# Kernel optimization log

Hardware: AMD Instinct MI355X
Metric: run time of the kernel (lower is better)

Reference implementation:

```python
import jax, jax.numpy as jnp
import numpy as np
from jax import lax

KERNEL = 3      # patch size
STRIDE = 1      # matching stride at low res
RATE = 2        # downsample rate
SOFTMAX_SCALE = 10.0


def _extract_patches(img, k, stride):
    """tf.image.extract_patches with SAME padding. img: [B,H,W,C] -> [B, oh*ow, k, k, C]."""
    B, H, W, C = img.shape
    oh = -(-H // stride)
    ow = -(-W // stride)
    ph = max((oh - 1) * stride + k - H, 0)
    pw = max((ow - 1) * stride + k - W, 0)
    img = jnp.pad(img, ((0, 0), (ph // 2, ph - ph // 2), (pw // 2, pw - pw // 2), (0, 0)))
    # stack the k*k shifted strided views; channel-last order matches TF's (kh, kw, C) flattening
    cols = [img[:, dh:dh + (oh - 1) * stride + 1:stride, dw:dw + (ow - 1) * stride + 1:stride, :]
            for dh in range(k) for dw in range(k)]
    p = jnp.stack(cols, axis=3)  # [B, oh, ow, k*k, C]
    return p.reshape(B, oh * ow, k, k, C)


def _avgpool2(x):
    """Exact equivalent of TF bilinear (antialias=False) downsample by factor 2."""
    B, H, W, C = x.shape
    return x.reshape(B, H // 2, 2, W // 2, 2, C).mean(axis=(2, 4))


def _conv_same(x4, w):
    return lax.conv_general_dilated(x4, w, (1, 1), 'SAME',
                                    dimension_numbers=('NHWC', 'HWIO', 'NHWC'))


def _forward(x, mask):
    B, H, W, C = x.shape
    k, stride, rate = KERNEL, STRIDE, RATE
    h, w = H // rate, W // rate
    L = h * w

    # raw (full-res) patches used for reconstruction: [B,k,k,C,L]
    raw_w = jnp.transpose(_extract_patches(x, k, rate * stride), (0, 2, 3, 4, 1))
    # low-res foreground / background (identical here, as in the source)
    f = _avgpool2(x)              # [B,h,w,C]
    m = _avgpool2(mask)           # [B,h,w,1]
    # low-res matching patches: [B,k,k,C,L]
    wp = jnp.transpose(_extract_patches(f, k, stride), (0, 2, 3, 4, 1))
    # mask patches -> gate: mm = 1 where the 3x3 mask patch mean is exactly 1.0
    mp = _extract_patches(m, k, stride)                       # [B,L,k,k,1]
    mm = (jnp.mean(mp, axis=(2, 3, 4)) == 1.0).astype(jnp.float32)  # [B,L]

    fuse_w = jnp.eye(KERNEL, dtype=jnp.float32).reshape(KERNEL, KERNEL, 1, 1)

    def per_item(xi, wi, rwi, mmi):
        # xi:[h,w,C]  wi,rwi:[k,k,C,L]  mmi:[L]
        wn = wi / jnp.maximum(jnp.sqrt(jnp.sum(wi * wi, axis=(0, 1, 2))), 1e-4)
        yi = _conv_same(xi[None], wn)          # [1,h,w,L] cosine-similarity logits
        att = yi[0]
        # fuse: diagonal conv over the [L,L] score matrix in both patch orderings
        z = yi.reshape(1, L, L, 1)
        z = _conv_same(z, fuse_w)
        z = z.reshape(1, h, w, h, w).transpose(0, 2, 1, 4, 3).reshape(1, L, L, 1)
        z = _conv_same(z, fuse_w)
        z = z.reshape(1, w, h, w, h).transpose(0, 2, 1, 4, 3)
        yi = z.reshape(1, h, w, L)
        mm4 = mmi.reshape(1, 1, 1, L)
        yi = jax.nn.softmax(yi * mm4 * SOFTMAX_SCALE, axis=3) * mm4
        # reconstruction: transposed conv with raw full-res patches as filters
        out = lax.conv_transpose(yi, rwi, (rate, rate), 'SAME',
                                 dimension_numbers=('NHWC', 'HWIO', 'NHWC'),
                                 transpose_kernel=True) / float(rate * rate)
        return out[0], att

    y, att = jax.vmap(per_item)(f, wp, raw_w, mm)
    return y, att


def setup_inputs() -> dict:
    key = jax.random.key(0)
    x = jax.random.normal(key, (2, 128, 128, 64), dtype=jnp.float32)
    # binary hole mask: ones inside a centered 64x64 square
    mask = jnp.zeros((2, 128, 128, 1), jnp.float32).at[:, 32:96, 32:96, :].set(1.0)
    return {"x": x, "mask": mask}


def reference(x, mask):
    return _forward(x, mask)
```

## Files before the change

kernel.cpp:

```cpp
#include <hip/hip_runtime.h>
#include <hip/hip_bf16.h>

typedef _Float16 f16x8 __attribute__((ext_vector_type(8)));
typedef float f32x4 __attribute__((ext_vector_type(4)));

__device__ __forceinline__ void gload_lds16(const void* gptr, void* lptr) {
  __builtin_amdgcn_global_load_lds(
      (const __attribute__((address_space(1))) void*)gptr,
      (__attribute__((address_space(3))) void*)lptr, 16, 0, 0);
}

__global__ __launch_bounds__(256) void k_pre(const float* __restrict__ x,
                                             const float* __restrict__ mask,
                                             _Float16* __restrict__ f_h,
                                             float* __restrict__ sumsq,
                                             float* __restrict__ mlow) {
  int wave = threadIdx.x >> 6, c = threadIdx.x & 63;
  int blk = blockIdx.x * 4 + wave;
  int b = blk >> 12, ij = blk & 4095;
  int i = ij >> 6, j = ij & 63;
  size_t base = ((size_t)(b * 128 + 2 * i) * 128 + 2 * j) * 64 + c;
  float f = 0.25f * (x[base] + x[base + 64] + x[base + 128 * 64] + x[base + 128 * 64 + 64]);
  f_h[(size_t)blk * 64 + c] = (_Float16)f;
  float fsq = f * f;
  for (int off = 32; off; off >>= 1) fsq += __shfl_down(fsq, off);
  if (c == 0) {
    sumsq[blk] = fsq;
    size_t mb = (size_t)(b * 128 + 2 * i) * 128 + 2 * j;
    mlow[blk] = 0.25f * (mask[mb] + mask[mb + 1] + mask[mb + 128] + mask[mb + 129]);
  }
}

__global__ __launch_bounds__(1024) void k_norm_compact(const float* __restrict__ sumsq,
                                                       const float* __restrict__ mlow,
                                                       float* __restrict__ invn,
                                                       int* __restrict__ actIdx,
                                                       int* __restrict__ nAct) {
  int b = blockIdx.x;
  int t = threadIdx.x;
  __shared__ unsigned char mmf[4096];
  for (int l = t; l < 4096; l += 1024) {
    int li = l >> 6, lj = l & 63;
    float s = 0.f;
    bool ok = true;
    for (int dh = -1; dh <= 1; ++dh)
      for (int dw = -1; dw <= 1; ++dw) {
        int ii = li + dh, jj = lj + dw;
        float mv = 0.f;
        if ((unsigned)ii < 64u && (unsigned)jj < 64u) {
          int idx = (b << 12) + ii * 64 + jj;
          s += sumsq[idx];
          mv = mlow[idx];
        }
        ok = ok && (mv == 1.0f);
      }
    invn[(b << 12) + l] = 1.0f / fmaxf(sqrtf(s), 1e-4f);
    mmf[l] = ok ? 1 : 0;
  }
  __syncthreads();
  int lane = t & 63, wv = t >> 6;
  __shared__ int wsum[16];
  __shared__ int sbase;
  if (t == 0) sbase = 0;
  __syncthreads();
  for (int chunk = 0; chunk < 4; ++chunk) {
    int l = chunk * 1024 + t;
    int flag = mmf[l] ? 1 : 0;
    unsigned long long m = __ballot(flag);
    int wpre = __popcll(m & ((1ull << lane) - 1ull));
    if (lane == 0) wsum[wv] = __popcll(m);
    __syncthreads();
    int off = sbase;
    for (int w2 = 0; w2 < wv; ++w2) off += wsum[w2];
    if (flag) {
      int pos = off + wpre;
      if (pos < 1024) actIdx[(b << 10) + pos] = l;
    }
    __syncthreads();
    if (t == 0) {
      int s2 = 0;
      for (int w2 = 0; w2 < 16; ++w2) s2 += wsum[w2];
      sbase += s2;
    }
    __syncthreads();
  }
  int total = sbase;
  if (t >= total) actIdx[(b << 10) + t] = 0;
  if (t == 0) nAct[b] = (total > 1024) ? 1024 : total;
}

__global__ __launch_bounds__(256) void k_build_p(const _Float16* __restrict__ f_h,
                                                 _Float16* __restrict__ P) {
  int wave = threadIdx.x >> 6, c = threadIdx.x & 63;
  int blk = blockIdx.x * 4 + wave;
  int b = blk >> 12, l = blk & 4095;
  int li = l >> 6, lj = l & 63;
  _Float16* dst = P + (size_t)blk * 576 + c;
#pragma unroll
  for (int kk = 0; kk < 9; ++kk) {
    int kh = kk / 3, kw = kk % 3;
    int ii = li + kh - 1, jj = lj + kw - 1;
    _Float16 v = (_Float16)0.f;
    if ((unsigned)ii < 64u && (unsigned)jj < 64u)
      v = f_h[((size_t)(b << 12) + ii * 64 + jj) * 64 + c];
    dst[kk * 64] = v;
  }
}

__global__ void k_build_rt(const float* __restrict__ x, _Float16* __restrict__ Rt) {
  int kh = blockIdx.x, li = blockIdx.y, b = blockIdx.z;
  int r = 2 * li + kh;
  __shared__ float xrow[128 * 65];
  if (r < 128) {
    for (int t = threadIdx.x; t < 8192; t += 256) {
      int v = t >> 6, c = t & 63;
      xrow[v * 65 + c] = x[((size_t)(b * 128 + r) * 128 + v) * 64 + c];
    }
  }
  __syncthreads();
  for (int idx = threadIdx.x; idx < 12288; idx += 256) {
    int lj = idx & 63, rest = idx >> 6;
    int c = rest & 63, kw = rest >> 6;
    int v = 2 * lj + kw;
    float val = (r < 128 && v < 128) ? xrow[v * 65 + c] : 0.f;
    int n = (kh * 3 + kw) * 64 + c;
    Rt[((size_t)b * 640 + n) * 4096 + li * 64 + lj] = (_Float16)val;
  }
}

__global__ void k_rtsub(const _Float16* __restrict__ Rt, const int* __restrict__ actIdx,
                        _Float16* __restrict__ Rts) {
  int n = blockIdx.x, b = blockIdx.y;
  const _Float16* src = Rt + ((size_t)b * 640 + n) * 4096;
  _Float16* dst = Rts + ((size_t)b * 640 + n) * 1024;
  const int* aIdx = actIdx + (b << 10);
  for (int s = threadIdx.x; s < 1024; s += 256) dst[s] = src[aIdx[s]];
}

__global__ __launch_bounds__(256) void k_gemm_sim(const _Float16* __restrict__ P,
                                                  const float* __restrict__ invn,
                                                  float* __restrict__ att) {
  int b = blockIdx.z;
  const _Float16* Ab = P + (size_t)b * 4096 * 576;
  int idx = blockIdx.x;
  int bj = (int)((sqrtf(8.f * (float)idx + 1.f) - 1.f) * 0.5f);
  while ((bj + 1) * (bj + 2) / 2 <= idx) ++bj;
  while (bj * (bj + 1) / 2 > idx) --bj;
  int bi = idx - bj * (bj + 1) / 2;
  int rowBase = bi * 128, colBase = bj * 128;
  bool diag = (bi == bj);

  __shared__ alignas(16) _Float16 As[128 * 64];
  __shared__ alignas(16) _Float16 Bs[128 * 64];
  __shared__ alignas(16) float tbuf[32][132];
  int tid = threadIdx.x, wave = tid >> 6, lane = tid & 63;
  int q = lane >> 4, rr = lane & 15;
  int wr = (wave >> 1) * 64, wc = (wave & 1) * 64;
  f32x4 acc[4][4] = {};
  for (int kt = 0; kt < 576; kt += 64) {
    __syncthreads();
#pragma unroll
    for (int t = 0; t < 4; ++t) {
      int chunk = t * 256 + wave * 64 + lane;
      int row = chunk >> 3;
      int kc = ((chunk & 7) ^ (row & 7)) * 8;
      gload_lds16(Ab + (size_t)(rowBase + row) * 576 + kt + kc,
                  As + (size_t)(t * 256 + wave * 64) * 8);
      if (!diag)
        gload_lds16(Ab + (size_t)(colBase + row) * 576 + kt + kc,
                    Bs + (size_t)(t * 256 + wave * 64) * 8);
    }
    __syncthreads();
    const _Float16* Bsrc = diag ? As : Bs;
#pragma unroll
    for (int ks = 0; ks < 2; ++ks) {
      f16x8 af[4], bf[4];
#pragma unroll
      for (int mi = 0; mi < 4; ++mi) {
        int r = wr + mi * 16 + rr;
        int ps = (ks * 4 + q) ^ (r & 7);
        af[mi] = *(const f16x8*)(As + r * 64 + ps * 8);
      }
#pragma unroll
      for (int ni = 0; ni < 4; ++ni) {
        int r = wc + ni * 16 + rr;
        int ps = (ks * 4 + q) ^ (r & 7);
        bf[ni] = *(const f16x8*)(Bsrc + r * 64 + ps * 8);
      }
#pragma unroll
      for (int mi = 0; mi < 4; ++mi)
#pragma unroll
        for (int ni = 0; ni < 4; ++ni)
          acc[mi][ni] = __builtin_amdgcn_mfma_f32_16x16x32_f16(af[mi], bf[ni], acc[mi][ni], 0, 0, 0);
    }
  }
  float* attb = att + ((size_t)b << 24);
#pragma unroll
  for (int ni = 0; ni < 4; ++ni) {
    int gc = colBase + wc + ni * 16 + rr;
    float sc = invn[(b << 12) + gc];
#pragma unroll
    for (int mi = 0; mi < 4; ++mi)
#pragma unroll
      for (int reg = 0; reg < 4; ++reg) {
        int gr = rowBase + wr + mi * 16 + q * 4 + reg;
        attb[((size_t)gr << 12) + gc] = acc[mi][ni][reg] * sc;
      }
  }
  if (diag) return;
  const float* ivrow = invn + (b << 12) + rowBase;
#pragma unroll
  for (int ph = 0; ph < 4; ++ph) {
    __syncthreads();
    if ((ph >> 1) == (wc >> 6)) {
      int nlo = (ph & 1) * 2;
#pragma unroll
      for (int nn = 0; nn < 2; ++nn) {
        int ni = nlo + nn;
        int rloc = nn * 16 + rr;
#pragma unroll
        for (int mi = 0; mi < 4; ++mi)
          *(f32x4*)&tbuf[rloc][wr + mi * 16 + q * 4] = acc[mi][ni];
      }
    }
    __syncthreads();
    int r = tid >> 3;
    int cbase = (tid & 7) * 16;
    int grow = colBase + ph * 32 + r;
    float* dst = attb + ((size_t)grow << 12) + rowBase + cbase;
#pragma unroll
    for (int cc = 0; cc < 16; cc += 4) {
      f32x4 v = *(f32x4*)&tbuf[r][cbase + cc];
      f32x4 s = *(const f32x4*)(ivrow + cbase + cc);
      *(f32x4*)(dst + cc) = v * s;
    }
  }
}

__global__ __launch_bounds__(256) void k_fuse_softmax3(const float* __restrict__ att,
                                                       const int* __restrict__ actIdx,
                                                       const int* __restrict__ nAct,
                                                       _Float16* __restrict__ Asub) {
  int blk0 = blockIdx.x;
  int blk = (blk0 & 7) * 1024 + (blk0 >> 3);
  int b = blk >> 12, p = blk & 4095;
  const float* Y = att + ((size_t)b << 24);
  const int* aIdx = actIdx + (b << 10);
  int na = nAct[b];
  int tid = threadIdx.x;
  int pi = p >> 6, pj = p & 63;
  int acol = pj * 64 + pi;

  int ls[4];
  bool act[4];
  float F[4] = {0.f, 0.f, 0.f, 0.f};
#pragma unroll
  for (int s4 = 0; s4 < 4; ++s4) {
    int slot = s4 * 256 + tid;
    ls[s4] = aIdx[slot];
    act[s4] = (slot < na);
  }

#pragma unroll
  for (int d2 = -1; d2 <= 1; ++d2) {
    int a2 = acol + d2;
    if ((unsigned)a2 >= 4096u) continue;
    int p2 = ((a2 & 63) << 6) | (a2 >> 6);
    int l2[4];
    bool lok[4];
#pragma unroll
    for (int s4 = 0; s4 < 4; ++s4) {
      int l = ls[s4];
      int bcol = ((l & 63) << 6) | (l >> 6);
      int b2 = bcol + d2;
      lok[s4] = act[s4] && ((unsigned)b2 < 4096u);
      int b2c = lok[s4] ? b2 : 0;
      l2[s4] = ((b2c & 63) << 6) | (b2c >> 6);
    }
#pragma unroll
    for (int d1 = -1; d1 <= 1; ++d1) {
      int qq = p2 + d1;
      if ((unsigned)qq >= 4096u) continue;
      const float* row = Y + ((size_t)qq << 12);
#pragma unroll
      for (int s4 = 0; s4 < 4; ++s4) {
        int rr2 = l2[s4] + d1;
        if (lok[s4] && (unsigned)rr2 < 4096u) F[s4] += row[rr2];
      }
    }
  }

  float z[4];
  float mx = (na < 4096) ? 0.f : -1e30f;
#pragma unroll
  for (int s4 = 0; s4 < 4; ++s4) {
    z[s4] = act[s4] ? F[s4] * 10.f : -1e30f;
    mx = fmaxf(mx, z[s4]);
  }
  __shared__ float red[4];
  for (int off = 32; off; off >>= 1) mx = fmaxf(mx, __shfl_down(mx, off));
  if ((tid & 63) == 0) red[tid >> 6] = mx;
  __syncthreads();
  mx = fmaxf(fmaxf(red[0], red[1]), fmaxf(red[2], red[3]));
  float e[4];
  float esum = 0.f;
#pragma unroll
  for (int s4 = 0; s4 < 4; ++s4) {
    e[s4] = act[s4] ? __expf(z[s4] - mx) : 0.f;
    esum += e[s4];
  }
  for (int off = 32; off; off >>= 1) esum += __shfl_down(esum, off);
  __syncthreads();
  if ((tid & 63) == 0) red[tid >> 6] = esum;
  __syncthreads();
  float total = red[0] + red[1] + red[2] + red[3] + (float)(4096 - na) * __expf(0.f - mx);
  float inv = 1.f / total;
  _Float16* Ap = Asub + ((size_t)blk << 10);
#pragma unroll
  for (int s4 = 0; s4 < 4; ++s4) Ap[s4 * 256 + tid] = (_Float16)(e[s4] * inv);
}

__global__ __launch_bounds__(256) void k_gemm_recon(const _Float16* __restrict__ Asub,
                                                    const _Float16* __restrict__ Rts,
                                                    float* __restrict__ y) {
  int b = blockIdx.z;
  const _Float16* Ab = Asub + ((size_t)b << 22);
  const _Float16* Bb = Rts + (size_t)b * 640 * 1024;
  int rowBase = blockIdx.y * 128, colBase = blockIdx.x * 128;
  __shared__ alignas(16) _Float16 As[128 * 64];
  __shared__ alignas(16) _Float16 Bs[128 * 64];
  int tid = threadIdx.x, wave = tid >> 6, lane = tid & 63;
  int q = lane >> 4, rr = lane & 15;
  int wr = (wave >> 1) * 64, wc = (wave & 1) * 64;
  f32x4 acc[4][4] = {};
  for (int kt = 0; kt < 1024; kt += 64) {
    __syncthreads();
#pragma unroll
    for (int t = 0; t < 4; ++t) {
      int chunk = t * 256 + wave * 64 + lane;
      int row = chunk >> 3;
      int kc = ((chunk & 7) ^ (row & 7)) * 8;
      gload_lds16(Ab + ((size_t)(rowBase + row) << 10) + kt + kc,
                  As + (size_t)(t * 256 + wave * 64) * 8);
      gload_lds16(Bb + ((size_t)(colBase + row) << 10) + kt + kc,
                  Bs + (size_t)(t * 256 + wave * 64) * 8);
    }
    __syncthreads();
#pragma unroll
    for (int ks = 0; ks < 2; ++ks) {
      f16x8 af[4], bf[4];
#pragma unroll
      for (int mi = 0; mi < 4; ++mi) {
        int r = wr + mi * 16 + rr;
        int ps = (ks * 4 + q) ^ (r & 7);
        af[mi] = *(const f16x8*)(As + r * 64 + ps * 8);
      }
#pragma unroll
      for (int ni = 0; ni < 4; ++ni) {
        int r = wc + ni * 16 + rr;
        int ps = (ks * 4 + q) ^ (r & 7);
        bf[ni] = *(const f16x8*)(Bs + r * 64 + ps * 8);
      }
#pragma unroll
      for (int mi = 0; mi < 4; ++mi)
#pragma unroll
        for (int ni = 0; ni < 4; ++ni)
          acc[mi][ni] = __builtin_amdgcn_mfma_f32_16x16x32_f16(af[mi], bf[ni], acc[mi][ni], 0, 0, 0);
    }
  }
#pragma unroll
  for (int ni = 0; ni < 4; ++ni) {
    int gc = colBase + wc + ni * 16 + rr;
    if (gc < 576) {
      int kk = gc >> 6, c = gc & 63;
      int kh = kk / 3, kw = kk - kh * 3;
#pragma unroll
      for (int mi = 0; mi < 4; ++mi)
#pragma unroll
        for (int reg = 0; reg < 4; ++reg) {
          int gp = rowBase + wr + mi * 16 + q * 4 + reg;
          int i = gp >> 6, j = gp & 63;
          int u = 2 * i + kh, v = 2 * j + kw;
          if (u < 128 && v < 128)
            atomicAdd(y + (((size_t)((b * 128 + u) * 128 + v)) << 6) + c,
                      0.25f * acc[mi][ni][reg]);
        }
    }
  }
}

extern "C" void kernel_launch(void* const* d_in, const int* in_sizes, int n_in,
                              void* d_out, int out_size, void* d_ws, size_t ws_size,
                              hipStream_t stream) {
  const float* x = (const float*)d_in[0];
  const float* mask = (const float*)d_in[1];
  float* out = (float*)d_out;
  float* y = out;
  float* att = out + 2097152;

  char* ws = (char*)d_ws;
  _Float16* f_h = (_Float16*)(ws + 0);
  float* sumsq = (float*)(ws + 0x100000);
  float* mlow = (float*)(ws + 0x108000);
  float* invn = (float*)(ws + 0x110000);
  _Float16* P = (_Float16*)(ws + 0x120000);
  _Float16* Rt = (_Float16*)(ws + 0xA20000);
  int* actIdx = (int*)(ws + 0x1420000);
  int* nAct = (int*)(ws + 0x1422000);
  _Float16* Rts = (_Float16*)(ws + 0x1430000);
  _Float16* Asub = (_Float16*)(ws + 0x16B0000);
  (void)in_sizes; (void)n_in; (void)out_size; (void)ws_size;

  hipMemsetAsync(y, 0, (size_t)2097152 * 4, stream);

  k_pre<<<2048, 256, 0, stream>>>(x, mask, f_h, sumsq, mlow);
  k_norm_compact<<<2, 1024, 0, stream>>>(sumsq, mlow, invn, actIdx, nAct);
  k_build_p<<<2048, 256, 0, stream>>>(f_h, P);
  k_build_rt<<<dim3(3, 64, 2), 256, 0, stream>>>(x, Rt);
  k_rtsub<<<dim3(640, 2), 256, 0, stream>>>(Rt, actIdx, Rts);
  k_gemm_sim<<<dim3(528, 1, 2), 256, 0, stream>>>(P, invn, att);
  k_fuse_softmax3<<<8192, 256, 0, stream>>>(att, actIdx, nAct, Asub);
  k_gemm_recon<<<dim3(5, 32, 2), 256, 0, stream>>>(Asub, Rts, y);
}
```

Measured before the change: 295.2 us.

## Merge prep kernels into fewer launches and batch four softmax rows per block

Combines k_pre with k_build_rt, and k_build_p with k_rtsub, into single launches that dispatch on block index. This cuts kernel launches from eight to six. The fused softmax kernel now processes four consecutive query rows per block with a loop, reusing the loaded active indices, and launches 2048 blocks instead of 8192. The cost is less parallelism per launch, extra block barriers inside the softmax loop, and the large shared-memory buffer from the Rt path now being allocated for every block of the merged prep kernel, which may lower its occupancy.

```diff
diff --git a/kernel.cpp b/kernel.cpp
--- a/kernel.cpp
+++ b/kernel.cpp
@@ -10,24 +10,49 @@
       (__attribute__((address_space(3))) void*)lptr, 16, 0, 0);
 }
 
-__global__ __launch_bounds__(256) void k_pre(const float* __restrict__ x,
+__global__ __launch_bounds__(256) void k_prt(const float* __restrict__ x,
                                              const float* __restrict__ mask,
                                              _Float16* __restrict__ f_h,
                                              float* __restrict__ sumsq,
-                                             float* __restrict__ mlow) {
-  int wave = threadIdx.x >> 6, c = threadIdx.x & 63;
-  int blk = blockIdx.x * 4 + wave;
-  int b = blk >> 12, ij = blk & 4095;
-  int i = ij >> 6, j = ij & 63;
-  size_t base = ((size_t)(b * 128 + 2 * i) * 128 + 2 * j) * 64 + c;
-  float f = 0.25f * (x[base] + x[base + 64] + x[base + 128 * 64] + x[base + 128 * 64 + 64]);
-  f_h[(size_t)blk * 64 + c] = (_Float16)f;
-  float fsq = f * f;
-  for (int off = 32; off; off >>= 1) fsq += __shfl_down(fsq, off);
-  if (c == 0) {
-    sumsq[blk] = fsq;
-    size_t mb = (size_t)(b * 128 + 2 * i) * 128 + 2 * j;
-    mlow[blk] = 0.25f * (mask[mb] + mask[mb + 1] + mask[mb + 128] + mask[mb + 129]);
+                                             float* __restrict__ mlow,
+                                             _Float16* __restrict__ Rt) {
+  if (blockIdx.x < 2048) {
+    int wave = threadIdx.x >> 6, c = threadIdx.x & 63;
+    int blk = blockIdx.x * 4 + wave;
+    int b = blk >> 12, ij = blk & 4095;
+    int i = ij >> 6, j = ij & 63;
+    size_t base = ((size_t)(b * 128 + 2 * i) * 128 + 2 * j) * 64 + c;
+    float f = 0.25f * (x[base] + x[base + 64] + x[base + 128 * 64] + x[base + 128 * 64 + 64]);
+    f_h[(size_t)blk * 64 + c] = (_Float16)f;
+    float fsq = f * f;
+    for (int off = 32; off; off >>= 1) fsq += __shfl_down(fsq, off);
+    if (c == 0) {
+      sumsq[blk] = fsq;
+      size_t mb = (size_t)(b * 128 + 2 * i) * 128 + 2 * j;
+      mlow[blk] = 0.25f * (mask[mb] + mask[mb + 1] + mask[mb + 128] + mask[mb + 129]);
+    }
+    return;
+  }
+  int idx = blockIdx.x - 2048;
+  int kh = idx % 3;
+  int rest = idx / 3;
+  int li = rest & 63, b = rest >> 6;
+  int r = 2 * li + kh;
+  __shared__ float xrow[128 * 65];
+  if (r < 128) {
+    for (int t = threadIdx.x; t < 8192; t += 256) {
+      int v = t >> 6, c = t & 63;
+      xrow[v * 65 + c] = x[((size_t)(b * 128 + r) * 128 + v) * 64 + c];
+    }
+  }
+  __syncthreads();
+  for (int id2 = threadIdx.x; id2 < 12288; id2 += 256) {
+    int lj = id2 & 63, rest2 = id2 >> 6;
+    int c = rest2 & 63, kw = rest2 >> 6;
+    int v = 2 * lj + kw;
+    float val = (r < 128 && v < 128) ? xrow[v * 65 + c] : 0.f;
+    int n = (kh * 3 + kw) * 64 + c;
+    Rt[((size_t)b * 640 + n) * 4096 + li * 64 + lj] = (_Float16)val;
   }
 }
 
@@ -89,48 +114,30 @@
   if (t == 0) nAct[b] = (total > 1024) ? 1024 : total;
 }
 
-__global__ __launch_bounds__(256) void k_build_p(const _Float16* __restrict__ f_h,
-                                                 _Float16* __restrict__ P) {
-  int wave = threadIdx.x >> 6, c = threadIdx.x & 63;
-  int blk = blockIdx.x * 4 + wave;
-  int b = blk >> 12, l = blk & 4095;
-  int li = l >> 6, lj = l & 63;
-  _Float16* dst = P + (size_t)blk * 576 + c;
-#pragma unroll
-  for (int kk = 0; kk < 9; ++kk) {
-    int kh = kk / 3, kw = kk % 3;
-    int ii = li + kh - 1, jj = lj + kw - 1;
-    _Float16 v = (_Float16)0.f;
-    if ((unsigned)ii < 64u && (unsigned)jj < 64u)
-      v = f_h[((size_t)(b << 12) + ii * 64 + jj) * 64 + c];
-    dst[kk * 64] = v;
-  }
-}
-
-__global__ void k_build_rt(const float* __restrict__ x, _Float16* __restrict__ Rt) {
-  int kh = blockIdx.x, li = blockIdx.y, b = blockIdx.z;
-  int r = 2 * li + kh;
-  __shared__ float xrow[128 * 65];
-  if (r < 128) {
-    for (int t = threadIdx.x; t < 8192; t += 256) {
-      int v = t >> 6, c = t & 63;
-      xrow[v * 65 + c] = x[((size_t)(b * 128 + r) * 128 + v) * 64 + c];
-    }
-  }
-  __syncthreads();
-  for (int idx = threadIdx.x; idx < 12288; idx += 256) {
-    int lj = idx & 63, rest = idx >> 6;
-    int c = rest & 63, kw = rest >> 6;
-    int v = 2 * lj + kw;
-    float val = (r < 128 && v < 128) ? xrow[v * 65 + c] : 0.f;
-    int n = (kh * 3 + kw) * 64 + c;
-    Rt[((size_t)b * 640 + n) * 4096 + li * 64 + lj] = (_Float16)val;
-  }
-}
-
-__global__ void k_rtsub(const _Float16* __restrict__ Rt, const int* __restrict__ actIdx,
-                        _Float16* __restrict__ Rts) {
-  int n = blockIdx.x, b = blockIdx.y;
+__global__ __launch_bounds__(256) void k_psub(const _Float16* __restrict__ f_h,
+                                              _Float16* __restrict__ P,
+                                              const _Float16* __restrict__ Rt,
+                                              const int* __restrict__ actIdx,
+                                              _Float16* __restrict__ Rts) {
+  if (blockIdx.x < 2048) {
+    int wave = threadIdx.x >> 6, c = threadIdx.x & 63;
+    int blk = blockIdx.x * 4 + wave;
+    int b = blk >> 12, l = blk & 4095;
+    int li = l >> 6, lj = l & 63;
+    _Float16* dst = P + (size_t)blk * 576 + c;
+#pragma unroll
+    for (int kk = 0; kk < 9; ++kk) {
+      int kh = kk / 3, kw = kk % 3;
+      int ii = li + kh - 1, jj = lj + kw - 1;
+      _Float16 v = (_Float16)0.f;
+      if ((unsigned)ii < 64u && (unsigned)jj < 64u)
+        v = f_h[((size_t)(b << 12) + ii * 64 + jj) * 64 + c];
+      dst[kk * 64] = v;
+    }
+    return;
+  }
+  int idx = blockIdx.x - 2048;
+  int n = idx % 640, b = idx / 640;
   const _Float16* src = Rt + ((size_t)b * 640 + n) * 4096;
   _Float16* dst = Rts + ((size_t)b * 640 + n) * 1024;
   const int* aIdx = actIdx + (b << 10);
@@ -237,87 +244,93 @@
   }
 }
 
-__global__ __launch_bounds__(256) void k_fuse_softmax3(const float* __restrict__ att,
+__global__ __launch_bounds__(256) void k_fuse_softmax6(const float* __restrict__ att,
                                                        const int* __restrict__ actIdx,
                                                        const int* __restrict__ nAct,
                                                        _Float16* __restrict__ Asub) {
-  int blk0 = blockIdx.x;
-  int blk = (blk0 & 7) * 1024 + (blk0 >> 3);
-  int b = blk >> 12, p = blk & 4095;
+  int g0 = blockIdx.x;
+  int g = (g0 & 7) * 256 + (g0 >> 3);
+  int b = g >> 10;
   const float* Y = att + ((size_t)b << 24);
   const int* aIdx = actIdx + (b << 10);
   int na = nAct[b];
   int tid = threadIdx.x;
-  int pi = p >> 6, pj = p & 63;
-  int acol = pj * 64 + pi;
 
   int ls[4];
   bool act[4];
-  float F[4] = {0.f, 0.f, 0.f, 0.f};
 #pragma unroll
   for (int s4 = 0; s4 < 4; ++s4) {
     int slot = s4 * 256 + tid;
     ls[s4] = aIdx[slot];
     act[s4] = (slot < na);
   }
-
-#pragma unroll
-  for (int d2 = -1; d2 <= 1; ++d2) {
-    int a2 = acol + d2;
-    if ((unsigned)a2 >= 4096u) continue;
-    int p2 = ((a2 & 63) << 6) | (a2 >> 6);
-    int l2[4];
-    bool lok[4];
+  __shared__ float red[4];
+  _Float16* Ap0 = Asub + ((size_t)g << 12);
+
+  for (int pp = 0; pp < 4; ++pp) {
+    int p = ((g & 1023) << 2) + pp;
+    int pi = p >> 6, pj = p & 63;
+    int acol = pj * 64 + pi;
+    float F[4] = {0.f, 0.f, 0.f, 0.f};
+
+#pragma unroll
+    for (int d2 = -1; d2 <= 1; ++d2) {
+      int a2 = acol + d2;
+      if ((unsigned)a2 >= 4096u) continue;
+      int p2 = ((a2 & 63) << 6) | (a2 >> 6);
+      int l2[4];
+      bool lok[4];
+#pragma unroll
+      for (int s4 = 0; s4 < 4; ++s4) {
+        int l = ls[s4];
+        int bcol = ((l & 63) << 6) | (l >> 6);
+        int b2 = bcol + d2;
+        lok[s4] = act[s4] && ((unsigned)b2 < 4096u);
+        int b2c = lok[s4] ? b2 : 0;
+        l2[s4] = ((b2c & 63) << 6) | (b2c >> 6);
+      }
+#pragma unroll
+      for (int d1 = -1; d1 <= 1; ++d1) {
+        int qq = p2 + d1;
+        if ((unsigned)qq >= 4096u) continue;
+        const float* row = Y + ((size_t)qq << 12);
+#pragma unroll
+        for (int s4 = 0; s4 < 4; ++s4) {
+          int rr2 = l2[s4] + d1;
+          if (lok[s4] && (unsigned)rr2 < 4096u) F[s4] += row[rr2];
+        }
+      }
+    }
+
+    float z[4];
+    float mx = (na < 4096) ? 0.f : -1e30f;
 #pragma unroll
     for (int s4 = 0; s4 < 4; ++s4) {
-      int l = ls[s4];
-      int bcol = ((l & 63) << 6) | (l >> 6);
-      int b2 = bcol + d2;
-      lok[s4] = act[s4] && ((unsigned)b2 < 4096u);
-      int b2c = lok[s4] ? b2 : 0;
-      l2[s4] = ((b2c & 63) << 6) | (b2c >> 6);
-    }
-#pragma unroll
-    for (int d1 = -1; d1 <= 1; ++d1) {
-      int qq = p2 + d1;
-      if ((unsigned)qq >= 4096u) continue;
-      const float* row = Y + ((size_t)qq << 12);
-#pragma unroll
-      for (int s4 = 0; s4 < 4; ++s4) {
-        int rr2 = l2[s4] + d1;
-        if (lok[s4] && (unsigned)rr2 < 4096u) F[s4] += row[rr2];
-      }
-    }
-  }
-
-  float z[4];
-  float mx = (na < 4096) ? 0.f : -1e30f;
-#pragma unroll
-  for (int s4 = 0; s4 < 4; ++s4) {
-    z[s4] = act[s4] ? F[s4] * 10.f : -1e30f;
-    mx = fmaxf(mx, z[s4]);
-  }
-  __shared__ float red[4];
-  for (int off = 32; off; off >>= 1) mx = fmaxf(mx, __shfl_down(mx, off));
-  if ((tid & 63) == 0) red[tid >> 6] = mx;
-  __syncthreads();
-  mx = fmaxf(fmaxf(red[0], red[1]), fmaxf(red[2], red[3]));
-  float e[4];
-  float esum = 0.f;
-#pragma unroll
-  for (int s4 = 0; s4 < 4; ++s4) {
-    e[s4] = act[s4] ? __expf(z[s4] - mx) : 0.f;
-    esum += e[s4];
-  }
-  for (int off = 32; off; off >>= 1) esum += __shfl_down(esum, off);
-  __syncthreads();
-  if ((tid & 63) == 0) red[tid >> 6] = esum;
-  __syncthreads();
-  float total = red[0] + red[1] + red[2] + red[3] + (float)(4096 - na) * __expf(0.f - mx);
-  float inv = 1.f / total;
-  _Float16* Ap = Asub + ((size_t)blk << 10);
-#pragma unroll
-  for (int s4 = 0; s4 < 4; ++s4) Ap[s4 * 256 + tid] = (_Float16)(e[s4] * inv);
+      z[s4] = act[s4] ? F[s4] * 10.f : -1e30f;
+      mx = fmaxf(mx, z[s4]);
+    }
+    for (int off = 32; off; off >>= 1) mx = fmaxf(mx, __shfl_down(mx, off));
+    if ((tid & 63) == 0) red[tid >> 6] = mx;
+    __syncthreads();
+    mx = fmaxf(fmaxf(red[0], red[1]), fmaxf(red[2], red[3]));
+    float e[4];
+    float esum = 0.f;
+#pragma unroll
+    for (int s4 = 0; s4 < 4; ++s4) {
+      e[s4] = act[s4] ? __expf(z[s4] - mx) : 0.f;
+      esum += e[s4];
+    }
+    for (int off = 32; off; off >>= 1) esum += __shfl_down(esum, off);
+    __syncthreads();
+    if ((tid & 63) == 0) red[tid >> 6] = esum;
+    __syncthreads();
+    float total = red[0] + red[1] + red[2] + red[3] + (float)(4096 - na) * __expf(0.f - mx);
+    float inv = 1.f / total;
+    _Float16* Ap = Ap0 + (pp << 10);
+#pragma unroll
+    for (int s4 = 0; s4 < 4; ++s4) Ap[s4 * 256 + tid] = (_Float16)(e[s4] * inv);
+    __syncthreads();
+  }
 }
 
 __global__ __launch_bounds__(256) void k_gemm_recon(const _Float16* __restrict__ Asub,
@@ -413,12 +426,10 @@
 
   hipMemsetAsync(y, 0, (size_t)2097152 * 4, stream);
 
-  k_pre<<<2048, 256, 0, stream>>>(x, mask, f_h, sumsq, mlow);
+  k_prt<<<2432, 256, 0, stream>>>(x, mask, f_h, sumsq, mlow, Rt);
   k_norm_compact<<<2, 1024, 0, stream>>>(sumsq, mlow, invn, actIdx, nAct);
-  k_build_p<<<2048, 256, 0, stream>>>(f_h, P);
-  k_build_rt<<<dim3(3, 64, 2), 256, 0, stream>>>(x, Rt);
-  k_rtsub<<<dim3(640, 2), 256, 0, stream>>>(Rt, actIdx, Rts);
+  k_psub<<<3328, 256, 0, stream>>>(f_h, P, Rt, actIdx, Rts);
   k_gemm_sim<<<dim3(528, 1, 2), 256, 0, stream>>>(P, invn, att);
-  k_fuse_softmax3<<<8192, 256, 0, stream>>>(att, actIdx, nAct, Asub);
+  k_fuse_softmax6<<<2048, 256, 0, stream>>>(att, actIdx, nAct, Asub);
   k_gemm_recon<<<dim3(5, 32, 2), 256, 0, stream>>>(Asub, Rts, y);
 }
```

New measurement: 328.7 us. 11.3% more time.
